# Kernel tuning notes

Hardware: AMD Instinct MI355X
Metric: run time of the kernel (lower is better)

Reference implementation:

```python
import jax, jax.numpy as jnp
import numpy as np

K = 5            # kernel_size per pseudo-dim
N = 51200        # nodes
E = 819200       # edges (avg degree 16)
B = 64           # graphs in batch

# 2^dim corner offsets for degree-1 (linear) open B-spline in dim=2
_BITS = jnp.array([[0, 0], [0, 1], [1, 0], [1, 1]], dtype=jnp.int32)  # [4,2]

def spline_basis(pseudo):
    # pseudo: [E,2] in [0,1]. Returns basis [E,4], weight indices [E,4].
    v = pseudo * (K - 1)
    lo = jnp.clip(jnp.floor(v).astype(jnp.int32), 0, K - 2)   # [E,2]
    frac = v - lo.astype(pseudo.dtype)                        # [E,2]
    idx = lo[:, None, :] + _BITS[None]                        # [E,4,2]
    w = jnp.where(_BITS[None] == 1, frac[:, None, :], 1.0 - frac[:, None, :])
    basis = w.prod(-1)                                        # [E,4]
    widx = idx[..., 0] * K + idx[..., 1]                      # [E,4] in [0,25)
    return basis, widx

def spline_conv(x, src, dst, basis, widx, W, root, bias):
    # x:[N,Fin], W:[25,Fin,Fout], root:[Fin,Fout], bias:[Fout]
    n = x.shape[0]
    Z = jnp.einsum('ni,kio->nko', x, W)          # [N,25,Fout] per-node per-kernel transforms
    Zg = Z[src[:, None], widx]                   # [E,4,Fout] irregular gather
    msg = jnp.einsum('es,eso->eo', basis, Zg)    # [E,Fout]
    agg = jax.ops.segment_sum(msg, dst, num_segments=n)
    deg = jax.ops.segment_sum(jnp.ones_like(msg[:, 0]), dst, num_segments=n)
    agg = agg / jnp.maximum(deg, 1.0)[:, None]   # mean aggregation
    return agg + x @ root + bias

def setup_inputs():
    key = jax.random.key(0)
    ks = jax.random.split(key, 12)
    x = jax.random.normal(ks[0], (N, 7), jnp.float32)
    edge_index = jax.random.randint(ks[1], (2, E), 0, N, dtype=jnp.int32)
    pseudo = jax.random.uniform(ks[2], (E, 2), jnp.float32)
    slices = jnp.arange(B + 1, dtype=jnp.int32) * (N // B)   # graph boundaries
    W1 = jax.random.normal(ks[3], (K * K, 7, 32), jnp.float32) * 0.2
    root1 = jax.random.normal(ks[4], (7, 32), jnp.float32) * 0.2
    b1 = jnp.zeros((32,), jnp.float32)
    W2 = jax.random.normal(ks[5], (K * K, 32, 64), jnp.float32) * 0.1
    root2 = jax.random.normal(ks[6], (32, 64), jnp.float32) * 0.1
    b2 = jnp.zeros((64,), jnp.float32)
    fc_w = jax.random.normal(ks[7], (64, 30), jnp.float32) * 0.1
    fc_b = jnp.zeros((30,), jnp.float32)
    return {"x": x, "edge_index": edge_index, "pseudo": pseudo, "slices": slices,
            "W1": W1, "root1": root1, "b1": b1, "W2": W2, "root2": root2,
            "b2": b2, "fc_w": fc_w, "fc_b": fc_b}

def reference(x, edge_index, pseudo, slices, W1, root1, b1, W2, root2, b2, fc_w, fc_b):
    src, dst = edge_index[0], edge_index[1]
    basis, widx = spline_basis(pseudo)
    h = jax.nn.elu(spline_conv(x, src, dst, basis, widx, W1, root1, b1))
    h = jax.nn.elu(spline_conv(h, src, dst, basis, widx, W2, root2, b2))
    # batch_average: mean of node features per graph (slices = boundaries)
    gid = jnp.clip(jnp.searchsorted(slices, jnp.arange(N), side='right') - 1, 0, B - 1)
    sums = jax.ops.segment_sum(h, gid, num_segments=B)
    counts = (slices[1:] - slices[:-1]).astype(h.dtype)
    g = sums / jnp.maximum(counts, 1.0)[:, None]             # [B,64]
    # dropout is identity in eval mode
    logits = g @ fc_w + fc_b
    return jax.nn.log_softmax(logits, axis=-1)
```

## Files before the change

### kernel.cpp

```cpp
#include <hip/hip_runtime.h>
#include <hip/hip_fp16.h>
#include <math.h>

#define N_NODES 51200
#define N_EDGES 819200
#define NB 64
#define CAP 64

typedef _Float16 half8 __attribute__((ext_vector_type(8)));
typedef __attribute__((ext_vector_type(4))) float float4v;

__device__ __forceinline__ float eluf(float x) {
  return x > 0.f ? x : expm1f(x);
}

__device__ __forceinline__ void dec2(int w0, int w1, int c, float& basf, int& Kc) {
  int K = w0 >> 16;
  float f0 = __half2float(__ushort_as_half((unsigned short)(w1 & 0xFFFF)));
  float f1 = __half2float(__ushort_as_half((unsigned short)(((unsigned)w1) >> 16)));
  float b0 = (c & 2) ? f0 : 1.f - f0;
  float bv = (c & 1) ? f1 : 1.f - f1;
  Kc = K + (c >> 1) * 5 + (c & 1);
  basf = b0 * bv;
}

__device__ __forceinline__ void rmw16(unsigned* Tr, int Kc, int q, float bf, int4 hv) {
  __half2 bas = __float2half2_rn(bf);
  __half2* tp = (__half2*)&Tr[Kc * 16 + q * 4];
  const __half2* h = (const __half2*)&hv;
  __half2 t0 = tp[0], t1 = tp[1], t2 = tp[2], t3 = tp[3];
  tp[0] = __hfma2(bas, h[0], t0);
  tp[1] = __hfma2(bas, h[1], t1);
  tp[2] = __hfma2(bas, h[2], t2);
  tp[3] = __hfma2(bas, h[3], t3);
}

__global__ __launch_bounds__(256) void prep_scatter(const int* __restrict__ ei,
                                                    const float* __restrict__ pseudo,
                                                    const float* __restrict__ x,
                                                    const float* __restrict__ W1,
                                                    const float* __restrict__ root1,
                                                    const float* __restrict__ W2,
                                                    const float* __restrict__ root2,
                                                    int* __restrict__ cnt,
                                                    int2* __restrict__ bucket,
                                                    __half* __restrict__ xh,
                                                    __half* __restrict__ W1T,
                                                    __half* __restrict__ W2T,
                                                    float* __restrict__ gbuf) {
  int b = blockIdx.x, tid = threadIdx.x;
  if (b < 400) {
    int base = b * 2048 + tid;
#pragma unroll
    for (int u = 0; u < 8; u++) {
      int e = base + u * 256;
      int src = ei[e], dst = ei[N_EDGES + e];
      float v0 = pseudo[2 * e] * 4.f;
      float v1 = pseudo[2 * e + 1] * 4.f;
      int lo0 = min(max((int)floorf(v0), 0), 3);
      int lo1 = min(max((int)floorf(v1), 0), 3);
      float f0 = v0 - (float)lo0, f1 = v1 - (float)lo1;
      int K = lo0 * 5 + lo1;
      unsigned short u0 = __half_as_ushort(__float2half(f0));
      unsigned short u1 = __half_as_ushort(__float2half(f1));
      int w0 = src | (K << 16);
      int w1 = (int)((unsigned)u0 | ((unsigned)u1 << 16));
      int slot = atomicAdd(&cnt[dst], 1);
      if (slot < CAP) bucket[(size_t)dst * CAP + slot] = make_int2(w0, w1);
    }
  } else if (b < 2000) {
    int idx = (b - 400) * 256 + tid;
    int n = idx >> 3, j = idx & 7;
    xh[idx] = __float2half((j < 7) ? x[n * 7 + j] : 0.f);
  } else if (b < 2028) {
    int idx = (b - 2000) * 256 + tid;
    int o = idx / 224, k = idx - o * 224;
    float v = 0.f;
    if (k < 200) {
      int cell = k >> 3, f = k & 7;
      if (f < 7) v = W1[(cell * 7 + f) * 32 + o];
    } else if (k < 207) {
      v = root1[(k - 200) * 32 + o];
    }
    if (idx < 7168) W1T[idx] = __float2half(v);
  } else if (b < 2236) {
    int idx = (b - 2028) * 256 + tid;
    int o = idx / 832, k = idx - o * 832;
    float v = (k < 800) ? W2[k * 64 + o] : root2[(k - 800) * 64 + o];
    W2T[idx] = __float2half(v);
  } else {
    int idx = (b - 2236) * 256 + tid;
    gbuf[idx] = 0.f;
  }
}

#define L1N 16
__global__ __launch_bounds__(256) void fused_l1(const int2* __restrict__ bucket,
                                                const int* __restrict__ cnt,
                                                const unsigned* __restrict__ xh,
                                                const __half* __restrict__ W1T,
                                                const float* __restrict__ b1,
                                                unsigned short* __restrict__ h1h) {
  __shared__ unsigned T[L1N * 112];
  __shared__ float invdeg_s[L1N];
  int tid = threadIdx.x;
  int n0 = blockIdx.x * L1N;
  for (int idx = tid; idx < L1N * 112; idx += 256) T[idx] = 0u;
  if (tid < L1N) invdeg_s[tid] = 1.f / fmaxf((float)cnt[n0 + tid], 1.f);
  __syncthreads();
  if (tid < L1N * 4) {
    int row = tid >> 2, p = tid & 3;
    int n = n0 + row;
    float dgc = fmaxf((float)cnt[n], 1.f);
    unsigned xv = xh[n * 4 + p];
    __half2 h = __hmul2(*(const __half2*)&xv, __float2half2_rn(dgc));
    T[row * 112 + 100 + p] = *(unsigned*)&h;
  }
  int wv = tid >> 6, l = tid & 63;
  int slot = l >> 4, c = (l >> 2) & 3, p = l & 3;
  int nn = wv * 4 + slot;
  int n = n0 + nn;
  int dg = min(cnt[n], CAP);
  int dmax = dg;
  dmax = max(dmax, __shfl_xor(dmax, 16));
  dmax = max(dmax, __shfl_xor(dmax, 32));
  const int2* bk = bucket + (size_t)n * CAP;
  unsigned* Tr = &T[nn * 112];
  int4 ra0 = *(const int4*)(bk + 0);
  int4 rb0 = *(const int4*)(bk + 2);
  int4 ra1 = *(const int4*)(bk + 4);
  int4 rb1 = *(const int4*)(bk + 6);
  unsigned xv0 = xh[(ra0.x & 0xFFFF) * 4 + p];
  unsigned xv1 = xh[(ra0.z & 0xFFFF) * 4 + p];
  unsigned xv2 = xh[(rb0.x & 0xFFFF) * 4 + p];
  unsigned xv3 = xh[(rb0.z & 0xFFFF) * 4 + p];
  for (int j = 0; j < dmax; j += 4) {
    int jp = min(j + 8, CAP - 4);
    int4 ra2 = *(const int4*)(bk + jp);
    int4 rb2 = *(const int4*)(bk + jp + 2);
    unsigned nx0 = xh[(ra1.x & 0xFFFF) * 4 + p];
    unsigned nx1 = xh[(ra1.z & 0xFFFF) * 4 + p];
    unsigned nx2 = xh[(rb1.x & 0xFFFF) * 4 + p];
    unsigned nx3 = xh[(rb1.z & 0xFFFF) * 4 + p];
    bool a0 = j < dg, a1 = j + 1 < dg, a2 = j + 2 < dg, a3 = j + 3 < dg;
    float bf; int Kc;
    if (a0) { dec2(ra0.x, ra0.y, c, bf, Kc);
      __half2* tp = (__half2*)&Tr[Kc * 4 + p];
      *tp = __hfma2(__float2half2_rn(bf), *(const __half2*)&xv0, *tp); }
    if (a1) { dec2(ra0.z, ra0.w, c, bf, Kc);
      __half2* tp = (__half2*)&Tr[Kc * 4 + p];
      *tp = __hfma2(__float2half2_rn(bf), *(const __half2*)&xv1, *tp); }
    if (a2) { dec2(rb0.x, rb0.y, c, bf, Kc);
      __half2* tp = (__half2*)&Tr[Kc * 4 + p];
      *tp = __hfma2(__float2half2_rn(bf), *(const __half2*)&xv2, *tp); }
    if (a3) { dec2(rb0.z, rb0.w, c, bf, Kc);
      __half2* tp = (__half2*)&Tr[Kc * 4 + p];
      *tp = __hfma2(__float2half2_rn(bf), *(const __half2*)&xv3, *tp); }
    ra0 = ra1; rb0 = rb1; ra1 = ra2; rb1 = rb2;
    xv0 = nx0; xv1 = nx1; xv2 = nx2; xv3 = nx3;
  }
  __syncthreads();
  if (wv < 2) {
    int m = l & 15, quad = l >> 4;
    const char* abase = (const char*)T + m * 448 + quad * 16;
    const __half* bbase = W1T + (wv * 16 + m) * 224 + quad * 8;
    float4v acc = {0.f, 0.f, 0.f, 0.f};
#pragma unroll
    for (int it = 0; it < 7; it++) {
      half8 af = *(const half8*)(abase + it * 64);
      half8 bf = *(const half8*)(bbase + it * 32);
      acc = __builtin_amdgcn_mfma_f32_16x16x32_f16(af, bf, acc, 0, 0, 0);
    }
    int feat = wv * 16 + m;
    float bb = b1[feat];
#pragma unroll
    for (int r = 0; r < 4; r++) {
      int row = quad * 4 + r;
      float v = eluf(acc[r] * invdeg_s[row] + bb);
      h1h[(size_t)(n0 + row) * 32 + feat] = __half_as_ushort(__float2half(v));
    }
  }
}

#define L2N 16
__global__ __launch_bounds__(256) void fused_l2(const int2* __restrict__ bucket,
                                                const int* __restrict__ cnt,
                                                const unsigned* __restrict__ h1hu,
                                                const __half* __restrict__ W2T,
                                                const float* __restrict__ b2,
                                                float* __restrict__ gbuf) {
  __shared__ unsigned T[L2N * 420];
  __shared__ float invdeg_s[L2N];
  int tid = threadIdx.x;
  int n0 = blockIdx.x * L2N;
  for (int idx = tid; idx < L2N * 420; idx += 256) T[idx] = 0u;
  if (tid < L2N) invdeg_s[tid] = 1.f / fmaxf((float)cnt[n0 + tid], 1.f);
  __syncthreads();
  {
    int row = tid >> 4, p = tid & 15;
    int n = n0 + row;
    float dgc = fmaxf((float)cnt[n], 1.f);
    unsigned hv = h1hu[(size_t)n * 16 + p];
    __half2 h = __hmul2(*(const __half2*)&hv, __float2half2_rn(dgc));
    T[row * 420 + 400 + p] = *(unsigned*)&h;
  }
  int wv = tid >> 6, l = tid & 63;
  int slot = l >> 4, c = (l >> 2) & 3, q = l & 3;
  int nn = wv * 4 + slot;
  int n = n0 + nn;
  int dg = min(cnt[n], CAP);
  int dmax = dg;
  dmax = max(dmax, __shfl_xor(dmax, 16));
  dmax = max(dmax, __shfl_xor(dmax, 32));
  const int2* bk = bucket + (size_t)n * CAP;
  unsigned* Tr = &T[nn * 420];
  const unsigned* h1q = h1hu + q * 4;
  int4 ra0 = *(const int4*)(bk + 0);
  int4 rb0 = *(const int4*)(bk + 2);
  int4 ra1 = *(const int4*)(bk + 4);
  int4 rb1 = *(const int4*)(bk + 6);
  int4 hv0 = *(const int4*)(h1q + (size_t)(ra0.x & 0xFFFF) * 16);
  int4 hv1 = *(const int4*)(h1q + (size_t)(ra0.z & 0xFFFF) * 16);
  int4 hv2 = *(const int4*)(h1q + (size_t)(rb0.x & 0xFFFF) * 16);
  int4 hv3 = *(const int4*)(h1q + (size_t)(rb0.z & 0xFFFF) * 16);
  for (int j = 0; j < dmax; j += 4) {
    int jp = min(j + 8, CAP - 4);
    int4 ra2 = *(const int4*)(bk + jp);
    int4 rb2 = *(const int4*)(bk + jp + 2);
    int4 nh0 = *(const int4*)(h1q + (size_t)(ra1.x & 0xFFFF) * 16);
    int4 nh1 = *(const int4*)(h1q + (size_t)(ra1.z & 0xFFFF) * 16);
    int4 nh2 = *(const int4*)(h1q + (size_t)(rb1.x & 0xFFFF) * 16);
    int4 nh3 = *(const int4*)(h1q + (size_t)(rb1.z & 0xFFFF) * 16);
    bool a0 = j < dg, a1 = j + 1 < dg, a2 = j + 2 < dg, a3 = j + 3 < dg;
    float bf; int Kc;
    if (a0) { dec2(ra0.x, ra0.y, c, bf, Kc); rmw16(Tr, Kc, q, bf, hv0); }
    if (a1) { dec2(ra0.z, ra0.w, c, bf, Kc); rmw16(Tr, Kc, q, bf, hv1); }
    if (a2) { dec2(rb0.x, rb0.y, c, bf, Kc); rmw16(Tr, Kc, q, bf, hv2); }
    if (a3) { dec2(rb0.z, rb0.w, c, bf, Kc); rmw16(Tr, Kc, q, bf, hv3); }
    ra0 = ra1; rb0 = rb1; ra1 = ra2; rb1 = rb2;
    hv0 = nh0; hv1 = nh1; hv2 = nh2; hv3 = nh3;
  }
  __syncthreads();
  int m = l & 15, quad = l >> 4;
  const char* abase = (const char*)T + m * 1680 + quad * 16;
  const __half* bbase = W2T + (size_t)(wv * 16 + m) * 832 + quad * 8;
  float4v acc = {0.f, 0.f, 0.f, 0.f};
  for (int it = 0; it < 26; it++) {
    half8 af = *(const half8*)(abase + it * 64);
    half8 bf = *(const half8*)(bbase + it * 32);
    acc = __builtin_amdgcn_mfma_f32_16x16x32_f16(af, bf, acc, 0, 0, 0);
  }
  int feat = wv * 16 + m;
  float bb = b2[feat];
  float psum = 0.f;
#pragma unroll
  for (int r = 0; r < 4; r++) {
    int node = quad * 4 + r;
    psum += eluf(acc[r] * invdeg_s[node] + bb);
  }
  psum += __shfl_xor(psum, 16);
  psum += __shfl_xor(psum, 32);
  if (l < 16) {
    int g = n0 / 800;
    atomicAdd(&gbuf[g * 64 + feat], psum);
  }
}

__global__ __launch_bounds__(64) void fc_ls(const float* __restrict__ gbuf,
                                            const int* __restrict__ slices,
                                            const float* __restrict__ fcw,
                                            const float* __restrict__ fcb,
                                            float* __restrict__ out) {
  int g = blockIdx.x;
  int l = threadIdx.x;
  float scale = 1.f / fmaxf((float)(slices[g + 1] - slices[g]), 1.f);
  float logit = -INFINITY;
  if (l < 30) {
    float acc = fcb[l];
    for (int i = 0; i < 64; i++) acc += gbuf[g * 64 + i] * scale * fcw[i * 30 + l];
    logit = acc;
  }
  float m = logit;
  for (int off = 16; off; off >>= 1) m = fmaxf(m, __shfl_xor(m, off, 32));
  float e = (l < 30) ? expf(logit - m) : 0.f;
  for (int off = 16; off; off >>= 1) e += __shfl_xor(e, off, 32);
  if (l < 30) out[g * 30 + l] = logit - m - logf(e);
}

extern "C" void kernel_launch(void* const* d_in, const int* in_sizes, int n_in,
                              void* d_out, int out_size, void* d_ws, size_t ws_size,
                              hipStream_t stream) {
  const float* x      = (const float*)d_in[0];
  const int*   ei     = (const int*)d_in[1];
  const float* pseudo = (const float*)d_in[2];
  const int*   slices = (const int*)d_in[3];
  const float* W1     = (const float*)d_in[4];
  const float* root1  = (const float*)d_in[5];
  const float* b1     = (const float*)d_in[6];
  const float* W2     = (const float*)d_in[7];
  const float* root2  = (const float*)d_in[8];
  const float* b2     = (const float*)d_in[9];
  const float* fcw    = (const float*)d_in[10];
  const float* fcb    = (const float*)d_in[11];
  float* out = (float*)d_out;

  char* ws = (char*)d_ws;
  int*      cnt    = (int*)ws;
  int2*     bucket = (int2*)(cnt + N_NODES);
  unsigned* h1h    = (unsigned*)(bucket + (size_t)N_NODES * CAP);
  float*    gbuf   = (float*)(h1h + (size_t)N_NODES * 16);
  unsigned* xh     = (unsigned*)(gbuf + 64 * 64);
  __half*   W1T    = (__half*)(xh + (size_t)N_NODES * 4);
  __half*   W2T    = W1T + 32 * 224;

  hipMemsetAsync(cnt, 0, N_NODES * sizeof(int), stream);

  prep_scatter<<<2252, 256, 0, stream>>>(ei, pseudo, x, W1, root1, W2, root2,
                                         cnt, bucket, (__half*)xh, W1T, W2T, gbuf);
  fused_l1<<<N_NODES / L1N, 256, 0, stream>>>(bucket, cnt, xh, W1T, b1,
                                              (unsigned short*)h1h);
  fused_l2<<<N_NODES / L2N, 256, 0, stream>>>(bucket, cnt, h1h, W2T, b2, gbuf);
  fc_ls<<<NB, 64, 0, stream>>>(gbuf, slices, fcw, fcb, out);
}
```

Before: 209.0 us.

## Sort nodes by degree within each graph to balance gather loops

Adds a small per-graph counting-sort kernel that builds a permutation of node ids ordered by in-degree. The two fused layer kernels then process nodes through this permutation, so the four nodes sharing a wavefront have similar degrees. This is meant to cut the idle iterations caused by looping to the wave-wide maximum degree. It costs an extra kernel launch, an indirection through perm, and scattered h1h row writes. Sorting stays within each 800-node graph, so blocks of 16 still map to a single graph for the pooled sums.

```diff
diff --git a/kernel.cpp b/kernel.cpp
--- a/kernel.cpp
+++ b/kernel.cpp
@@ -94,23 +94,51 @@
   }
 }
 
+__global__ __launch_bounds__(256) void sort_nodes(const int* __restrict__ cnt,
+                                                  int* __restrict__ perm) {
+  __shared__ int hist[65];
+  __shared__ int base[65];
+  int g = blockIdx.x, tid = threadIdx.x;
+  if (tid < 65) hist[tid] = 0;
+  __syncthreads();
+  for (int i = tid; i < 800; i += 256)
+    atomicAdd(&hist[min(cnt[g * 800 + i], 64)], 1);
+  __syncthreads();
+  if (tid == 0) {
+    int s = 0;
+    for (int b = 0; b < 65; b++) { base[b] = s; s += hist[b]; }
+  }
+  __syncthreads();
+  for (int i = tid; i < 800; i += 256) {
+    int nid = g * 800 + i;
+    int pos = atomicAdd(&base[min(cnt[nid], 64)], 1);
+    perm[g * 800 + pos] = nid;
+  }
+}
+
 #define L1N 16
 __global__ __launch_bounds__(256) void fused_l1(const int2* __restrict__ bucket,
                                                 const int* __restrict__ cnt,
+                                                const int* __restrict__ perm,
                                                 const unsigned* __restrict__ xh,
                                                 const __half* __restrict__ W1T,
                                                 const float* __restrict__ b1,
                                                 unsigned short* __restrict__ h1h) {
   __shared__ unsigned T[L1N * 112];
   __shared__ float invdeg_s[L1N];
+  __shared__ int nid_s[L1N];
   int tid = threadIdx.x;
   int n0 = blockIdx.x * L1N;
   for (int idx = tid; idx < L1N * 112; idx += 256) T[idx] = 0u;
-  if (tid < L1N) invdeg_s[tid] = 1.f / fmaxf((float)cnt[n0 + tid], 1.f);
+  if (tid < L1N) {
+    int nid = perm[n0 + tid];
+    nid_s[tid] = nid;
+    invdeg_s[tid] = 1.f / fmaxf((float)cnt[nid], 1.f);
+  }
   __syncthreads();
   if (tid < L1N * 4) {
     int row = tid >> 2, p = tid & 3;
-    int n = n0 + row;
+    int n = nid_s[row];
     float dgc = fmaxf((float)cnt[n], 1.f);
     unsigned xv = xh[n * 4 + p];
     __half2 h = __hmul2(*(const __half2*)&xv, __float2half2_rn(dgc));
@@ -119,7 +147,7 @@
   int wv = tid >> 6, l = tid & 63;
   int slot = l >> 4, c = (l >> 2) & 3, p = l & 3;
   int nn = wv * 4 + slot;
-  int n = n0 + nn;
+  int n = nid_s[nn];
   int dg = min(cnt[n], CAP);
   int dmax = dg;
   dmax = max(dmax, __shfl_xor(dmax, 16));
@@ -177,7 +205,7 @@
     for (int r = 0; r < 4; r++) {
       int row = quad * 4 + r;
       float v = eluf(acc[r] * invdeg_s[row] + bb);
-      h1h[(size_t)(n0 + row) * 32 + feat] = __half_as_ushort(__float2half(v));
+      h1h[(size_t)nid_s[row] * 32 + feat] = __half_as_ushort(__float2half(v));
     }
   }
 }
@@ -185,20 +213,26 @@
 #define L2N 16
 __global__ __launch_bounds__(256) void fused_l2(const int2* __restrict__ bucket,
                                                 const int* __restrict__ cnt,
+                                                const int* __restrict__ perm,
                                                 const unsigned* __restrict__ h1hu,
                                                 const __half* __restrict__ W2T,
                                                 const float* __restrict__ b2,
                                                 float* __restrict__ gbuf) {
   __shared__ unsigned T[L2N * 420];
   __shared__ float invdeg_s[L2N];
+  __shared__ int nid_s[L2N];
   int tid = threadIdx.x;
   int n0 = blockIdx.x * L2N;
   for (int idx = tid; idx < L2N * 420; idx += 256) T[idx] = 0u;
-  if (tid < L2N) invdeg_s[tid] = 1.f / fmaxf((float)cnt[n0 + tid], 1.f);
+  if (tid < L2N) {
+    int nid = perm[n0 + tid];
+    nid_s[tid] = nid;
+    invdeg_s[tid] = 1.f / fmaxf((float)cnt[nid], 1.f);
+  }
   __syncthreads();
   {
     int row = tid >> 4, p = tid & 15;
-    int n = n0 + row;
+    int n = nid_s[row];
     float dgc = fmaxf((float)cnt[n], 1.f);
     unsigned hv = h1hu[(size_t)n * 16 + p];
     __half2 h = __hmul2(*(const __half2*)&hv, __float2half2_rn(dgc));
@@ -207,7 +241,7 @@
   int wv = tid >> 6, l = tid & 63;
   int slot = l >> 4, c = (l >> 2) & 3, q = l & 3;
   int nn = wv * 4 + slot;
-  int n = n0 + nn;
+  int n = nid_s[nn];
   int dg = min(cnt[n], CAP);
   int dmax = dg;
   dmax = max(dmax, __shfl_xor(dmax, 16));
@@ -312,13 +346,15 @@
   unsigned* xh     = (unsigned*)(gbuf + 64 * 64);
   __half*   W1T    = (__half*)(xh + (size_t)N_NODES * 4);
   __half*   W2T    = W1T + 32 * 224;
+  int*      perm   = (int*)(W2T + 64 * 832);
 
   hipMemsetAsync(cnt, 0, N_NODES * sizeof(int), stream);
 
   prep_scatter<<<2252, 256, 0, stream>>>(ei, pseudo, x, W1, root1, W2, root2,
                                          cnt, bucket, (__half*)xh, W1T, W2T, gbuf);
-  fused_l1<<<N_NODES / L1N, 256, 0, stream>>>(bucket, cnt, xh, W1T, b1,
+  sort_nodes<<<NB, 256, 0, stream>>>(cnt, perm);
+  fused_l1<<<N_NODES / L1N, 256, 0, stream>>>(bucket, cnt, perm, xh, W1T, b1,
                                               (unsigned short*)h1h);
-  fused_l2<<<N_NODES / L2N, 256, 0, stream>>>(bucket, cnt, h1h, W2T, b2, gbuf);
+  fused_l2<<<N_NODES / L2N, 256, 0, stream>>>(bucket, cnt, perm, h1h, W2T, b2, gbuf);
   fc_ls<<<NB, 64, 0, stream>>>(gbuf, slices, fcw, fcb, out);
 }
```

New measurement: 210.4 us. About the same (+0.7%).
